# Performance work log

Measured on AMD Instinct MI355X. Metric: run time of the kernel, lower is better.

## Reference

```python
import jax, jax.numpy as jnp
import numpy as np

L, B, I, H = 1024, 128, 256, 512

def setup_inputs() -> dict:
    key = jax.random.key(0)
    k1, k2, k3, k4, k5 = jax.random.split(key, 5)
    s_i = 1.0 / np.sqrt(I)
    s_h = 1.0 / np.sqrt(H)
    return {
        "x": jax.random.normal(k1, (L, B, I), dtype=jnp.float32),
        "h": jax.random.normal(k2, (B, H), dtype=jnp.float32),
        "Wx": jax.random.uniform(k3, (H, I), jnp.float32, -s_i, s_i),
        "Wh": jax.random.uniform(k4, (H, H), jnp.float32, -s_h, s_h),
        "bh": jax.random.uniform(k5, (H,), jnp.float32, -s_h, s_h),
    }

def reference(x, h, Wx, Wh, bh):
    # Precompute input projection for all timesteps as one big GEMM:
    # (L,B,I) @ (I,H) -> (L,B,H)
    xproj = jnp.einsum("lbi,hi->lbh", x, Wx)

    def step(h_prev, xp_t):
        h_new = jnp.tanh(xp_t + h_prev @ Wh.T + bh)  # (B,H)
        return h_new, h_new

    _, h_seq = jax.lax.scan(step, h, xproj)
    return h_seq  # (L, B, H)
```

## Files before the change

kernel.cpp:

```cpp
#include <hip/hip_runtime.h>

#define L_DIM 1024
#define B_DIM 128
#define I_DIM 256
#define H_DIM 512

typedef unsigned short u16x8 __attribute__((ext_vector_type(8)));
typedef __bf16 bf16x8 __attribute__((ext_vector_type(8)));
typedef float f32x4 __attribute__((ext_vector_type(4)));
typedef unsigned long long u64;
typedef unsigned int u32;
typedef u64 u64x2 __attribute__((ext_vector_type(2)));

static __device__ __forceinline__ unsigned short f2bf(float f) {
  unsigned u = __builtin_bit_cast(unsigned, f);
  u += 0x7FFFu + ((u >> 16) & 1u);
  return (unsigned short)(u >> 16);
}
static __device__ __forceinline__ float bf2f(unsigned short b) {
  return __builtin_bit_cast(float, ((unsigned)b) << 16);
}
static __device__ __forceinline__ bf16x8 ld_frag_g(const unsigned short* p, size_t idx8) {
  return __builtin_bit_cast(bf16x8, reinterpret_cast<const u16x8*>(p)[idx8]);
}

__global__ void pack_weights(const float* __restrict__ Wx, const float* __restrict__ Wh,
                             unsigned short* __restrict__ WxHi, unsigned short* __restrict__ WxLo,
                             unsigned short* __restrict__ WhHi, unsigned short* __restrict__ WhLo) {
  int tid = blockIdx.x * blockDim.x + threadIdx.x;
  if (tid < 32 * 8 * 64) {
    int lane = tid & 63, kt = (tid >> 6) & 7, nt = tid >> 9;
    int n = nt * 16 + (lane & 15), k0 = kt * 32 + (lane >> 4) * 8;
    const float* src = Wx + (size_t)n * I_DIM + k0;
    #pragma unroll
    for (int j = 0; j < 8; ++j) {
      float v = src[j];
      unsigned short hb = f2bf(v);
      WxHi[(size_t)tid * 8 + j] = hb;
      WxLo[(size_t)tid * 8 + j] = f2bf(v - bf2f(hb));
    }
  }
  if (tid < 32 * 16 * 64) {
    int lane = tid & 63, kt = (tid >> 6) & 15, nt = tid >> 10;
    int n = nt * 16 + (lane & 15), k0 = kt * 32 + (lane >> 4) * 8;
    const float* src = Wh + (size_t)n * H_DIM + k0;
    #pragma unroll
    for (int j = 0; j < 8; ++j) {
      float v = src[j];
      unsigned short hb = f2bf(v);
      WhHi[(size_t)tid * 8 + j] = hb;
      WhLo[(size_t)tid * 8 + j] = f2bf(v - bf2f(hb));
    }
  }
}

__global__ __launch_bounds__(256) void xproj_kernel(const float* __restrict__ x,
    const unsigned short* __restrict__ WxHi, const unsigned short* __restrict__ WxLo,
    const float* __restrict__ bh, float* __restrict__ out) {
  __shared__ unsigned short ahi[128][40];
  __shared__ unsigned short alo[128][40];
  const int tid = threadIdx.x, lane = tid & 63, wid = tid >> 6;
  const int mbase = blockIdx.x * 128, cbase = blockIdx.y * 128;
  const int wrow = (wid >> 1) * 64, wcol = (wid & 1) * 64;
  f32x4 acc[4][4] = {};
  const int srow = tid >> 1, shalf = (tid & 1) * 16;

  for (int kt = 0; kt < 8; ++kt) {
    const f32x4* src = reinterpret_cast<const f32x4*>(
        x + (size_t)(mbase + srow) * I_DIM + kt * 32 + shalf);
    f32x4 v[4];
    v[0] = src[0]; v[1] = src[1]; v[2] = src[2]; v[3] = src[3];
    u16x8 hh[2], ll[2];
    #pragma unroll
    for (int q = 0; q < 2; ++q) {
      #pragma unroll
      for (int e = 0; e < 8; ++e) {
        float f = v[q * 2 + (e >> 2)][e & 3];
        unsigned short hb = f2bf(f);
        hh[q][e] = hb;
        ll[q][e] = f2bf(f - bf2f(hb));
      }
    }
    __syncthreads();
    *reinterpret_cast<u16x8*>(&ahi[srow][shalf]) = hh[0];
    *reinterpret_cast<u16x8*>(&ahi[srow][shalf + 8]) = hh[1];
    *reinterpret_cast<u16x8*>(&alo[srow][shalf]) = ll[0];
    *reinterpret_cast<u16x8*>(&alo[srow][shalf + 8]) = ll[1];
    __syncthreads();

    bf16x8 amh[4], aml[4];
    #pragma unroll
    for (int m = 0; m < 4; ++m) {
      amh[m] = __builtin_bit_cast(bf16x8, *reinterpret_cast<const u16x8*>(
          &ahi[wrow + m * 16 + (lane & 15)][(lane >> 4) * 8]));
      aml[m] = __builtin_bit_cast(bf16x8, *reinterpret_cast<const u16x8*>(
          &alo[wrow + m * 16 + (lane & 15)][(lane >> 4) * 8]));
    }
    bf16x8 bhh[4], bll[4];
    #pragma unroll
    for (int n = 0; n < 4; ++n) {
      int ntg = (cbase + wcol) / 16 + n;
      size_t idx = (size_t)(ntg * 8 + kt) * 64 + lane;
      bhh[n] = ld_frag_g(WxHi, idx);
      bll[n] = ld_frag_g(WxLo, idx);
    }
    #pragma unroll
    for (int m = 0; m < 4; ++m) {
      #pragma unroll
      for (int n = 0; n < 4; ++n) {
        acc[m][n] = __builtin_amdgcn_mfma_f32_16x16x32_bf16(amh[m], bhh[n], acc[m][n], 0, 0, 0);
        acc[m][n] = __builtin_amdgcn_mfma_f32_16x16x32_bf16(aml[m], bhh[n], acc[m][n], 0, 0, 0);
        acc[m][n] = __builtin_amdgcn_mfma_f32_16x16x32_bf16(amh[m], bll[n], acc[m][n], 0, 0, 0);
      }
    }
  }

  #pragma unroll
  for (int n = 0; n < 4; ++n) {
    int col = cbase + wcol + n * 16 + (lane & 15);
    float bv = bh[col];
    #pragma unroll
    for (int m = 0; m < 4; ++m) {
      int rg = mbase + wrow + m * 16 + ((lane >> 4) << 2);
      #pragma unroll
      for (int r = 0; r < 4; ++r)
        out[(size_t)(rg + r) * H_DIM + col] = acc[m][n][r] + bv;
    }
  }
}

__global__ __launch_bounds__(64, 1) void rnn_kernel(const float* __restrict__ h0,
    const unsigned short* __restrict__ WhHi, const unsigned short* __restrict__ WhLo,
    u32* __restrict__ ctr, unsigned short* __restrict__ slab,
    float* __restrict__ out) {
  const int lane = threadIdx.x & 63;
  const int b = blockIdx.x;
  const int g = b & 7, cw = (b >> 3) & 31;

  bf16x8 wfh[16], wfl[16];
  #pragma unroll
  for (int kt = 0; kt < 16; ++kt) {
    size_t idx = (size_t)(cw * 16 + kt) * 64 + lane;
    wfh[kt] = ld_frag_g(WhHi, idx);
    wfl[kt] = ld_frag_g(WhLo, idx);
  }

  const int arow = lane & 15;
  const int aoff = (lane >> 4) * 8;
  const int drow = (lane >> 4) * 4;
  const int gcol = cw * 16 + (lane & 15);

  bf16x8 af[16];
  #pragma unroll
  for (int kt = 0; kt < 16; ++kt) {
    const f32x4* hp = reinterpret_cast<const f32x4*>(
        h0 + (size_t)(g * 16 + arow) * H_DIM + kt * 32 + aoff);
    f32x4 v0 = hp[0], v1 = hp[1];
    u16x8 hv;
    #pragma unroll
    for (int e = 0; e < 4; ++e) { hv[e] = f2bf(v0[e]); hv[4 + e] = f2bf(v1[e]); }
    af[kt] = __builtin_bit_cast(bf16x8, hv);
  }

  f32x4 xpA, xpB;
  #pragma unroll
  for (int r = 0; r < 4; ++r)
    xpA[r] = out[(size_t)(g * 16 + drow + r) * H_DIM + gcol];
  #pragma unroll
  for (int r = 0; r < 4; ++r)
    xpB[r] = out[(size_t)B_DIM * H_DIM + (size_t)(g * 16 + drow + r) * H_DIM + gcol];

  for (int t = 0; t < L_DIM; ++t) {
    const size_t obase = ((size_t)t * B_DIM + g * 16) * H_DIM;

    f32x4 a0 = {}, a1 = {}, a2 = {}, a3 = {};
    #pragma unroll
    for (int kt = 0; kt < 16; kt += 2) {
      a0 = __builtin_amdgcn_mfma_f32_16x16x32_bf16(af[kt], wfh[kt], a0, 0, 0, 0);
      a1 = __builtin_amdgcn_mfma_f32_16x16x32_bf16(af[kt], wfl[kt], a1, 0, 0, 0);
      a2 = __builtin_amdgcn_mfma_f32_16x16x32_bf16(af[kt + 1], wfh[kt + 1], a2, 0, 0, 0);
      a3 = __builtin_amdgcn_mfma_f32_16x16x32_bf16(af[kt + 1], wfl[kt + 1], a3, 0, 0, 0);
    }

    float hv[4]; unsigned short hu[4];
    #pragma unroll
    for (int r = 0; r < 4; ++r) {
      float z = a0[r] + a1[r] + a2[r] + a3[r] + xpA[r];
      float e = __expf(2.0f * z);
      hv[r] = 1.0f - 2.0f / (e + 1.0f);
      hu[r] = f2bf(hv[r]);
    }

    if (t == L_DIM - 1) {
      #pragma unroll
      for (int r = 0; r < 4; ++r)
        out[obase + (size_t)(drow + r) * H_DIM + gcol] = hv[r];
      break;
    }

    const unsigned step = (unsigned)(t + 1);
    const unsigned buf = step & 1;
    unsigned short* sg = slab + (size_t)(buf * 8 + g) * 8192;
    u32* cp = ctr + (size_t)(buf * 8 + g) * 16;

    #pragma unroll
    for (int r = 0; r < 4; ++r)
      __hip_atomic_store(&sg[(drow + r) * H_DIM + gcol], hu[r],
                         __ATOMIC_RELAXED, __HIP_MEMORY_SCOPE_AGENT);
    __builtin_amdgcn_sched_barrier(0);
    asm volatile("s_waitcnt vmcnt(0)" ::: "memory");
    __builtin_amdgcn_sched_barrier(0);
    if (lane == 0)
      __hip_atomic_fetch_add(cp, 1u, __ATOMIC_RELAXED, __HIP_MEMORY_SCOPE_AGENT);

    #pragma unroll
    for (int r = 0; r < 4; ++r)
      out[obase + (size_t)(drow + r) * H_DIM + gcol] = hv[r];
    xpA = xpB;
    {
      const int tn = (t + 2 < L_DIM) ? t + 2 : L_DIM - 1;
      const size_t obn = ((size_t)tn * B_DIM + g * 16) * H_DIM;
      #pragma unroll
      for (int r = 0; r < 4; ++r)
        xpB[r] = out[obn + (size_t)(drow + r) * H_DIM + gcol];
    }

    const u32 target = 32u * ((step + 1) >> 1);
    while (__hip_atomic_load(cp, __ATOMIC_RELAXED, __HIP_MEMORY_SCOPE_AGENT) < target) {}
    __builtin_amdgcn_sched_barrier(0);
    asm volatile("" ::: "memory");

    const u64* sp = reinterpret_cast<const u64*>(sg);
    #pragma unroll
    for (int kt = 0; kt < 16; ++kt) {
      const u64* p = sp + arow * 128 + kt * 8 + (lane >> 4) * 2;
      u64x2 pv2;
      pv2[0] = __hip_atomic_load(p, __ATOMIC_RELAXED, __HIP_MEMORY_SCOPE_AGENT);
      pv2[1] = __hip_atomic_load(p + 1, __ATOMIC_RELAXED, __HIP_MEMORY_SCOPE_AGENT);
      af[kt] = __builtin_bit_cast(bf16x8, pv2);
    }
  }
}

extern "C" void kernel_launch(void* const* d_in, const int* in_sizes, int n_in,
                              void* d_out, int out_size, void* d_ws, size_t ws_size,
                              hipStream_t stream) {
  (void)in_sizes; (void)n_in; (void)out_size; (void)ws_size;
  const float* x  = (const float*)d_in[0];
  const float* h0 = (const float*)d_in[1];
  const float* Wx = (const float*)d_in[2];
  const float* Wh = (const float*)d_in[3];
  const float* bh = (const float*)d_in[4];
  float* out = (float*)d_out;

  unsigned short* WxHi = (unsigned short*)d_ws;
  unsigned short* WxLo = WxHi + 131072;
  unsigned short* WhHi = WxLo + 131072;
  unsigned short* WhLo = WhHi + 262144;
  unsigned short* slab = (unsigned short*)((char*)d_ws + 1572864);
  u32*            ctr  = (u32*)((char*)d_ws + 1835008);

  hipMemsetAsync(ctr, 0, 1024, stream);

  hipLaunchKernelGGL(pack_weights, dim3(128), dim3(256), 0, stream,
                     Wx, Wh, WxHi, WxLo, WhHi, WhLo);
  hipLaunchKernelGGL(xproj_kernel, dim3(1024, 4), dim3(256), 0, stream,
                     x, WxHi, WxLo, bh, out);
  hipLaunchKernelGGL(rnn_kernel, dim3(256), dim3(64), 0, stream,
                     h0, WhHi, WhLo, ctr, slab, out);
}
```

Before: 3.261 ms.

## Share recurrent hidden-state slab across four waves through LDS per block

```diff
diff --git a/kernel.cpp b/kernel.cpp
--- a/kernel.cpp
+++ b/kernel.cpp
@@ -129,38 +129,35 @@
   }
 }
 
-__global__ __launch_bounds__(64, 1) void rnn_kernel(const float* __restrict__ h0,
+__global__ __launch_bounds__(256, 1) void rnn_kernel(const float* __restrict__ h0,
     const unsigned short* __restrict__ WhHi, const unsigned short* __restrict__ WhLo,
     u32* __restrict__ ctr, unsigned short* __restrict__ slab,
     float* __restrict__ out) {
-  const int lane = threadIdx.x & 63;
-  const int b = blockIdx.x;
-  const int g = b & 7, cw = (b >> 3) & 31;
-
-  bf16x8 wfh[16], wfl[16];
-  #pragma unroll
-  for (int kt = 0; kt < 16; ++kt) {
-    size_t idx = (size_t)(cw * 16 + kt) * 64 + lane;
-    wfh[kt] = ld_frag_g(WhHi, idx);
-    wfl[kt] = ld_frag_g(WhLo, idx);
-  }
+  __shared__ __attribute__((aligned(16))) unsigned short hb[2][16 * 520];
+  const int tid = threadIdx.x, lane = tid & 63, w = tid >> 6;
+  const int g = blockIdx.x & 7, c = blockIdx.x >> 3;
+  const int cw = c * 4 + w;
 
   const int arow = lane & 15;
   const int aoff = (lane >> 4) * 8;
   const int drow = (lane >> 4) * 4;
   const int gcol = cw * 16 + (lane & 15);
-
-  bf16x8 af[16];
-  #pragma unroll
-  for (int kt = 0; kt < 16; ++kt) {
-    const f32x4* hp = reinterpret_cast<const f32x4*>(
-        h0 + (size_t)(g * 16 + arow) * H_DIM + kt * 32 + aoff);
-    f32x4 v0 = hp[0], v1 = hp[1];
-    u16x8 hv;
-    #pragma unroll
-    for (int e = 0; e < 4; ++e) { hv[e] = f2bf(v0[e]); hv[4 + e] = f2bf(v1[e]); }
-    af[kt] = __builtin_bit_cast(bf16x8, hv);
-  }
+  const int prow = tid & 15;
+  const int pch  = tid >> 4;
+
+  {
+    const float* src = h0 + (size_t)(g * 16 + prow) * H_DIM + pch * 32;
+    #pragma unroll
+    for (int q = 0; q < 4; ++q) {
+      f32x4 v0 = reinterpret_cast<const f32x4*>(src)[2 * q];
+      f32x4 v1 = reinterpret_cast<const f32x4*>(src)[2 * q + 1];
+      u16x8 hv;
+      #pragma unroll
+      for (int e = 0; e < 4; ++e) { hv[e] = f2bf(v0[e]); hv[4 + e] = f2bf(v1[e]); }
+      *reinterpret_cast<u16x8*>(&hb[0][prow * 520 + pch * 32 + q * 8]) = hv;
+    }
+  }
+  __syncthreads();
 
   f32x4 xpA, xpB;
   #pragma unroll
@@ -172,14 +169,23 @@
 
   for (int t = 0; t < L_DIM; ++t) {
     const size_t obase = ((size_t)t * B_DIM + g * 16) * H_DIM;
+    const int cur = t & 1;
 
     f32x4 a0 = {}, a1 = {}, a2 = {}, a3 = {};
     #pragma unroll
     for (int kt = 0; kt < 16; kt += 2) {
-      a0 = __builtin_amdgcn_mfma_f32_16x16x32_bf16(af[kt], wfh[kt], a0, 0, 0, 0);
-      a1 = __builtin_amdgcn_mfma_f32_16x16x32_bf16(af[kt], wfl[kt], a1, 0, 0, 0);
-      a2 = __builtin_amdgcn_mfma_f32_16x16x32_bf16(af[kt + 1], wfh[kt + 1], a2, 0, 0, 0);
-      a3 = __builtin_amdgcn_mfma_f32_16x16x32_bf16(af[kt + 1], wfl[kt + 1], a3, 0, 0, 0);
+      bf16x8 af0 = __builtin_bit_cast(bf16x8, *reinterpret_cast<const u16x8*>(
+          &hb[cur][arow * 520 + kt * 32 + aoff]));
+      bf16x8 af1 = __builtin_bit_cast(bf16x8, *reinterpret_cast<const u16x8*>(
+          &hb[cur][arow * 520 + (kt + 1) * 32 + aoff]));
+      bf16x8 bh0 = ld_frag_g(WhHi, (size_t)(cw * 16 + kt) * 64 + lane);
+      bf16x8 bl0 = ld_frag_g(WhLo, (size_t)(cw * 16 + kt) * 64 + lane);
+      bf16x8 bh1 = ld_frag_g(WhHi, (size_t)(cw * 16 + kt + 1) * 64 + lane);
+      bf16x8 bl1 = ld_frag_g(WhLo, (size_t)(cw * 16 + kt + 1) * 64 + lane);
+      a0 = __builtin_amdgcn_mfma_f32_16x16x32_bf16(af0, bh0, a0, 0, 0, 0);
+      a1 = __builtin_amdgcn_mfma_f32_16x16x32_bf16(af0, bl0, a1, 0, 0, 0);
+      a2 = __builtin_amdgcn_mfma_f32_16x16x32_bf16(af1, bh1, a2, 0, 0, 0);
+      a3 = __builtin_amdgcn_mfma_f32_16x16x32_bf16(af1, bl1, a3, 0, 0, 0);
     }
 
     float hv[4]; unsigned short hu[4];
@@ -230,15 +236,23 @@
     __builtin_amdgcn_sched_barrier(0);
     asm volatile("" ::: "memory");
 
-    const u64* sp = reinterpret_cast<const u64*>(sg);
-    #pragma unroll
-    for (int kt = 0; kt < 16; ++kt) {
-      const u64* p = sp + arow * 128 + kt * 8 + (lane >> 4) * 2;
-      u64x2 pv2;
-      pv2[0] = __hip_atomic_load(p, __ATOMIC_RELAXED, __HIP_MEMORY_SCOPE_AGENT);
-      pv2[1] = __hip_atomic_load(p + 1, __ATOMIC_RELAXED, __HIP_MEMORY_SCOPE_AGENT);
-      af[kt] = __builtin_bit_cast(bf16x8, pv2);
-    }
+    const u64* pb = reinterpret_cast<const u64*>(sg) + prow * 128 + pch * 8;
+    u64 pl[8];
+    #pragma unroll
+    for (int j = 0; j < 8; ++j)
+      pl[j] = __hip_atomic_load(pb + j, __ATOMIC_RELAXED, __HIP_MEMORY_SCOPE_AGENT);
+
+    #pragma unroll
+    for (int q = 0; q < 4; ++q) {
+      u64x2 v2; v2[0] = pl[2 * q]; v2[1] = pl[2 * q + 1];
+      *reinterpret_cast<u64x2*>(&hb[buf][prow * 520 + pch * 32 + q * 8]) =
+          v2;
+    }
+    __builtin_amdgcn_sched_barrier(0);
+    asm volatile("s_waitcnt lgkmcnt(0)" ::: "memory");
+    __builtin_amdgcn_sched_barrier(0);
+    __builtin_amdgcn_s_barrier();
+    __builtin_amdgcn_sched_barrier(0);
   }
 }
 
@@ -266,6 +280,6 @@
                      Wx, Wh, WxHi, WxLo, WhHi, WhLo);
   hipLaunchKernelGGL(xproj_kernel, dim3(1024, 4), dim3(256), 0, stream,
                      x, WxHi, WxLo, bh, out);
-  hipLaunchKernelGGL(rnn_kernel, dim3(256), dim3(64), 0, stream,
+  hipLaunchKernelGGL(rnn_kernel, dim3(64), dim3(256), 0, stream,
                      h0, WhHi, WhLo, ctr, slab, out);
 }
```

After: 3.666 ms. +12.4%, slower.
